# Kernel optimization log

Measured on AMD Instinct MI355X. Metric: run time of the kernel, lower is better.

The kernel has to match this reference:

```python
import jax, jax.numpy as jnp
import numpy as np

BATCH, SEQ, D_MODEL = 4, 4096, 1024
HEADS, DIM_HEAD = 8, 128
BUCKET, N_HASHES = 64, 4
N_BUCKETS = SEQ // BUCKET
LN_EPS = 1e-3
SELF_ATTN_VAL = -5e4   # TOKEN_SELF_ATTN_VALUE in reformer_pytorch
MASK_VAL = -1e9        # stand-in for max_neg_value on padded keys
UNIT_EPS = 1e-6        # make_unit_length epsilon


def setup_inputs() -> dict:
    key = jax.random.key(0)
    ks = jax.random.split(key, 8)
    s = 0.02
    return {
        "i": jax.random.normal(ks[0], (BATCH, SEQ, D_MODEL), jnp.float32),
        "mask": jnp.ones((BATCH, SEQ), dtype=bool),
        "rotations": jax.random.normal(ks[1], (DIM_HEAD, N_HASHES, N_BUCKETS // 2), jnp.float32),
        "Wqk": jax.random.normal(ks[2], (D_MODEL, D_MODEL), jnp.float32) * s,
        "Wv": jax.random.normal(ks[3], (D_MODEL, D_MODEL), jnp.float32) * s,
        "Wo": jax.random.normal(ks[4], (D_MODEL, D_MODEL), jnp.float32) * s,
        "bo": jnp.zeros((D_MODEL,), jnp.float32),
        "ln_g": jnp.ones((D_MODEL,), jnp.float32),
        "ln_b": jnp.zeros((D_MODEL,), jnp.float32),
    }


def _look_one_back(x):
    # concat each chunk with the previous chunk along the within-chunk axis
    return jnp.concatenate([x, jnp.roll(x, 1, axis=1)], axis=2)


def _lsh_attention(qk, v, mask, rotations):
    # qk, v: (B, T, d) with B = batch*heads; mask: (B, T) bool
    B, T, d = qk.shape
    # --- hash into buckets (no grad through hashing) ---
    rot = jnp.einsum('btd,dhr->bhtr', jax.lax.stop_gradient(qk), rotations)
    rot = jnp.concatenate([rot, -rot], axis=-1)              # (B, nh, T, n_buckets)
    buckets = jnp.argmax(rot, axis=-1)                       # (B, nh, T)
    offsets = (jnp.arange(N_HASHES) * N_BUCKETS)[None, :, None]
    buckets = (buckets + offsets).reshape(B, N_HASHES * T)
    # --- stable bucket sort of tokens ---
    ticker = jnp.arange(N_HASHES * T)
    buckets_and_t = buckets * T + (ticker % T)               # unique keys
    sticker = jnp.argsort(buckets_and_t, axis=-1)            # (B, nh*T)
    undo_sort = jnp.argsort(sticker, axis=-1)
    st = sticker % T                                         # original positions
    sqk = jnp.take_along_axis(qk, st[..., None], axis=1)
    sv = jnp.take_along_axis(v, st[..., None], axis=1)
    # --- chunked local attention ---
    n_chunks = N_HASHES * N_BUCKETS
    bq_t = st.reshape(B, n_chunks, BUCKET)
    bq = sqk.reshape(B, n_chunks, BUCKET, d)
    nrm = jnp.linalg.norm(bq, axis=-1, keepdims=True)
    bk = bq / jnp.maximum(nrm, UNIT_EPS)                     # shared-QK: keys are unit-length queries
    bv = sv.reshape(B, n_chunks, BUCKET, d)
    bk = _look_one_back(bk)                                  # (B, C, 2*BUCKET, d)
    bv = _look_one_back(bv)
    bkv_t = _look_one_back(bq_t)                             # (B, C, 2*BUCKET)
    dots = jnp.einsum('bcid,bcjd->bcij', bq, bk) * (d ** -0.5)
    # input (padding) mask
    mq = jnp.take_along_axis(mask, st, axis=1).reshape(B, n_chunks, BUCKET)
    mkv = _look_one_back(mq)
    dots = jnp.where(mq[..., :, None] & mkv[..., None, :], dots, MASK_VAL)
    # avoid attending to self except as a fallback
    dots = jnp.where(bq_t[..., :, None] == bkv_t[..., None, :], SELF_ATTN_VAL, dots)
    dots_lse = jax.nn.logsumexp(dots, axis=-1, keepdims=True)  # (B, C, BUCKET, 1)
    probs = jnp.exp(dots - dots_lse)
    bo = jnp.einsum('bcij,bcjd->bcid', probs, bv)
    so = bo.reshape(B, N_HASHES * T, d)
    slogits = dots_lse.reshape(B, N_HASHES * T)
    # --- unsort and combine hash rounds via softmax over per-round logsumexps ---
    o = jnp.take_along_axis(so, undo_sort[..., None], axis=1).reshape(B, N_HASHES, T, d)
    logits = jnp.take_along_axis(slogits, undo_sort, axis=1).reshape(B, N_HASHES, T, 1)
    w = jnp.exp(logits - jax.nn.logsumexp(logits, axis=1, keepdims=True))
    return jnp.sum(o * w, axis=1)                            # (B, T, d)


def _forward(i, mask, rotations, Wqk, Wv, Wo, bo, ln_g, ln_b):
    b, t, dm = i.shape
    qk = i @ Wqk
    v = i @ Wv

    def split_heads(x):
        return x.reshape(b, t, HEADS, DIM_HEAD).transpose(0, 2, 1, 3).reshape(b * HEADS, t, DIM_HEAD)

    qk, v = split_heads(qk), split_heads(v)
    m = jnp.repeat(mask, HEADS, axis=0)                      # (b*h, t)
    out = _lsh_attention(qk, v, m, rotations)
    out = out.reshape(b, HEADS, t, DIM_HEAD).transpose(0, 2, 1, 3).reshape(b, t, dm)
    out = out @ Wo + bo                                      # to_out
    # eval-mode dropout is identity; then LayerNorm(eps=1e-3)
    mu = out.mean(-1, keepdims=True)
    var = out.var(-1, keepdims=True)
    return (out - mu) / jnp.sqrt(var + LN_EPS) * ln_g + ln_b


def reference(i, mask, rotations, Wqk, Wv, Wo, bo, ln_g, ln_b):
    return _forward(i, mask, rotations, Wqk, Wv, Wo, bo, ln_g, ln_b)
```

## Files before the change

### kernel.cpp

```cpp
#include <hip/hip_runtime.h>
#include <hip/hip_bf16.h>

#define B_   4
#define T_   4096
#define DM   1024
#define H_   8
#define DH   128
#define BHN  32
#define NH   4
#define NB   64
#define NT   16384
#define NC   256
#define SCALE_ 0.08838834764831845f
#define SELF_VAL -50000.0f
#define FLAG_CAP 262144
#define GAP_THR 2.5e-3f

typedef unsigned short u16;
typedef __attribute__((ext_vector_type(8))) short short8;
typedef __attribute__((ext_vector_type(8))) unsigned short us8;
typedef __attribute__((ext_vector_type(4))) float f32x4;

__device__ __forceinline__ float bf2f(u16 x) {
  union { unsigned u; float f; } c; c.u = ((unsigned)x) << 16; return c.f;
}
__device__ __forceinline__ u16 f2bf(float f) {
  union { float f; unsigned u; } c; c.f = f;
  unsigned r = (c.u + 0x7FFFu + ((c.u >> 16) & 1u)) >> 16;
  return (u16)r;
}
__device__ __forceinline__ void gload16(const void* g, void* l) {
  __builtin_amdgcn_global_load_lds(
      (const __attribute__((address_space(1))) void*)g,
      (__attribute__((address_space(3))) void*)l, 16, 0, 0);
}

__global__ __launch_bounds__(256) void k_isplit(
    const float* __restrict__ I, u16* __restrict__ ih, u16* __restrict__ il) {
  size_t idx = ((size_t)blockIdx.x * 256 + threadIdx.x) * 8;
  us8 vh, vl;
  #pragma unroll
  for (int e = 0; e < 8; ++e) {
    float x = I[idx + e];
    u16 h = f2bf(x);
    vh[e] = h;
    vl[e] = f2bf(x - bf2f(h));
  }
  *(us8*)(ih + idx) = vh;
  *(us8*)(il + idx) = vl;
}

__global__ __launch_bounds__(256) void k_wr(
    const float* __restrict__ Wqk, const float* __restrict__ R, double* __restrict__ WR) {
  __shared__ float lR[128][128];
  int tid = threadIdx.x;
  int k0 = blockIdx.x * 64, h = blockIdx.y;
  #pragma unroll
  for (int q = 0; q < 64; ++q)
    ((float*)lR)[q * 256 + tid] = R[q * 256 + tid];
  __syncthreads();
  int k = k0 + (tid >> 2);
  int hr0 = (tid & 3) * 32;
  double acc[32];
  #pragma unroll
  for (int j = 0; j < 32; ++j) acc[j] = 0.0;
  for (int d = 0; d < 128; ++d) {
    double w = (double)Wqk[(size_t)k * DM + h * DH + d];
    #pragma unroll
    for (int j = 0; j < 32; ++j)
      acc[j] = fma(w, (double)lR[d][hr0 + j], acc[j]);
  }
  double* o = WR + ((size_t)h * 1024 + k) * 128 + hr0;
  #pragma unroll
  for (int j = 0; j < 32; ++j) o[j] = acc[j];
}

__global__ __launch_bounds__(256) void k_wsplit(
    const float* __restrict__ Wqk, const float* __restrict__ Wv,
    const float* __restrict__ Wo, const double* __restrict__ WR,
    u16* __restrict__ Wqkvt, u16* __restrict__ Wot, u16* __restrict__ WR2t) {
  int tid = blockIdx.x * 256 + threadIdx.x;
  int k = tid >> 7, n8 = (tid & 127) << 3;
  #pragma unroll
  for (int j = 0; j < 8; ++j) {
    int n = n8 + j;
    Wqkvt[(size_t)n * 1024 + k]          = f2bf(Wqk[(size_t)k * 1024 + n]);
    Wqkvt[(size_t)(1024 + n) * 1024 + k] = f2bf(Wv [(size_t)k * 1024 + n]);
    Wot  [(size_t)n * 1024 + k]          = f2bf(Wo [(size_t)k * 1024 + n]);
    double w = WR[((size_t)(n >> 7) * 1024 + k) * 128 + (n & 127)];
    u16 wh = f2bf((float)w);
    u16 wl = f2bf((float)(w - (double)bf2f(wh)));
    WR2t[(size_t)n * 2048 + k] = wh;
    WR2t[(size_t)n * 2048 + 1024 + k] = wl;
  }
}

__global__ void k_zero(unsigned* flagc) { if (threadIdx.x == 0) *flagc = 0; }

template <int EPI>
__global__ __launch_bounds__(256) void k_gemm(
    const u16* __restrict__ A, const u16* __restrict__ A2,
    const u16* __restrict__ Bt,
    u16* __restrict__ outb, u16* __restrict__ outb2,
    float* __restrict__ outf, const float* __restrict__ bias,
    int* __restrict__ buckets, unsigned* __restrict__ flagc, int* __restrict__ flags) {
  __shared__ char smem[34816];
  u16 (*smA)[64] = (u16 (*)[64])smem;
  u16 (*smB)[64] = (u16 (*)[64])(smem + 16384);
  int tid = threadIdx.x;
  int m0 = blockIdx.x * 128, n0 = blockIdx.y * 128;
  int w = tid >> 6, lane = tid & 63;
  int wr = w >> 1, wc = w & 1;
  int arow = lane & 15, kg = lane >> 4;
  const int ldb = (EPI == 2) ? 2048 : 1024;
  int lrow = lane >> 3;
  int gch = (lane & 7) ^ lrow;

  f32x4 acc[4][4];
  #pragma unroll
  for (int m = 0; m < 4; ++m)
    #pragma unroll
    for (int n = 0; n < 4; ++n) acc[m][n] = (f32x4){0.f, 0.f, 0.f, 0.f};

  int axor = (arow & 7) << 3;

  auto run_seg = [&](const u16* Ab, const u16* Bb) {
    for (int kk = 0; kk < 1024; kk += 64) {
      __syncthreads();
      #pragma unroll
      for (int q = 0; q < 4; ++q) {
        int row = q * 32 + w * 8 + lrow;
        gload16(Ab + (size_t)(m0 + row) * 1024 + kk + gch * 8,
                smem + (q * 4096 + w * 1024));
        gload16(Bb + (size_t)(n0 + row) * ldb + kk + gch * 8,
                smem + 16384 + (q * 4096 + w * 1024));
      }
      __syncthreads();
      #pragma unroll
      for (int ks = 0; ks < 2; ++ks) {
        short8 af[4], bf[4];
        #pragma unroll
        for (int m = 0; m < 4; ++m)
          af[m] = *(const short8*)(&smA[wr * 64 + m * 16 + arow][((ks * 4 + kg) << 3) ^ axor]);
        #pragma unroll
        for (int n = 0; n < 4; ++n)
          bf[n] = *(const short8*)(&smB[wc * 64 + n * 16 + arow][((ks * 4 + kg) << 3) ^ axor]);
        #pragma unroll
        for (int m = 0; m < 4; ++m)
          #pragma unroll
          for (int n = 0; n < 4; ++n)
            acc[m][n] = __builtin_amdgcn_mfma_f32_16x16x32_bf16(af[m], bf[n], acc[m][n], 0, 0, 0);
      }
    }
  };

  if constexpr (EPI == 2) {
    run_seg(A, Bt);
    run_seg(A, Bt + 1024);
    run_seg(A2, Bt);
  } else {
    run_seg(A, Bt);
  }

  if constexpr (EPI == 0) {
    u16* dst = (n0 < 1024) ? outb : outb2;
    int nc0 = (n0 < 1024) ? n0 : (n0 - 1024);
    #pragma unroll
    for (int m = 0; m < 4; ++m)
      #pragma unroll
      for (int n = 0; n < 4; ++n)
        #pragma unroll
        for (int r = 0; r < 4; ++r) {
          int orow = wr * 64 + m * 16 + kg * 4 + r;
          int ocol = wc * 64 + n * 16 + arow;
          dst[(size_t)(m0 + orow) * 1024 + nc0 + ocol] = f2bf(acc[m][n][r]);
        }
  } else if constexpr (EPI == 1) {
    #pragma unroll
    for (int m = 0; m < 4; ++m)
      #pragma unroll
      for (int n = 0; n < 4; ++n)
        #pragma unroll
        for (int r = 0; r < 4; ++r) {
          int orow = wr * 64 + m * 16 + kg * 4 + r;
          int ocol = wc * 64 + n * 16 + arow;
          outf[(size_t)(m0 + orow) * 1024 + n0 + ocol] = acc[m][n][r] + bias[n0 + ocol];
        }
  } else {
    float (*sC)[132] = (float (*)[132])smem;
    #pragma unroll
    for (int pass = 0; pass < 2; ++pass) {
      __syncthreads();
      if (wr == pass) {
        #pragma unroll
        for (int m = 0; m < 4; ++m)
          #pragma unroll
          for (int n = 0; n < 4; ++n)
            #pragma unroll
            for (int r = 0; r < 4; ++r)
              sC[m * 16 + kg * 4 + r][wc * 64 + n * 16 + arow] = acc[m][n][r];
      }
      __syncthreads();
      int tok = tid >> 2, hash = tid & 3;
      const float* rw = &sC[tok][hash * 32];
      float m1 = -3.4e38f, m2 = -3.4e38f; int bi = 0;
      #pragma unroll
      for (int j = 0; j < 32; ++j) {
        float vv = rw[j];
        if (vv > m1) { m2 = m1; m1 = vv; bi = j; }
        else if (vv > m2) m2 = vv;
      }
      #pragma unroll
      for (int j = 0; j < 32; ++j) {
        float vv = -rw[j];
        if (vv > m1) { m2 = m1; m1 = vv; bi = 32 + j; }
        else if (vv > m2) m2 = vv;
      }
      int bt = m0 + pass * 64 + tok;
      int b = bt >> 12, t = bt & 4095;
      buckets[((size_t)(b * 8 + blockIdx.y) * 4 + hash) * T_ + t] = bi;
      if (m1 - m2 < GAP_THR) {
        unsigned pos = atomicAdd(flagc, 1u);
        if (pos < FLAG_CAP) flags[pos] = (bt << 5) | ((int)blockIdx.y << 2) | hash;
      }
    }
  }
}

__global__ __launch_bounds__(64) void k_fb(
    const float* __restrict__ I, const double* __restrict__ WR,
    const unsigned* __restrict__ flagc, const int* __restrict__ flags,
    int* __restrict__ buckets) {
  unsigned n = *flagc; if (n > FLAG_CAP) n = FLAG_CAP;
  int lane = threadIdx.x;
  for (unsigned it = blockIdx.x; it < n; it += gridDim.x) {
    int f = flags[it];
    int bt = f >> 5, h = (f >> 2) & 7, hash = f & 3;
    int j = lane & 31, half = lane >> 5;
    const float* ip = I + (size_t)bt * 1024 + half * 512;
    const double* wp = WR + ((size_t)h * 1024 + half * 512) * 128 + hash * 32 + j;
    double acc = 0.0;
    for (int k = 0; k < 512; ++k)
      acc = fma((double)ip[k], wp[(size_t)k * 128], acc);
    acc += __shfl_down(acc, 32, 64);
    double bv = acc; int bi = j;
    double vneg = -acc;
    if (vneg > bv) { bv = vneg; bi = 32 + j; }
    #pragma unroll
    for (int m = 1; m < 32; m <<= 1) {
      double ov = __shfl_xor(bv, m, 64);
      int oi = __shfl_xor(bi, m, 64);
      if (ov > bv || (ov == bv && oi < bi)) { bv = ov; bi = oi; }
    }
    if (lane == 0) {
      int b = bt >> 12, t = bt & 4095;
      buckets[((size_t)(b * 8 + h) * 4 + hash) * T_ + t] = bi;
    }
  }
}

__global__ __launch_bounds__(64) void k_sort(
    const int* __restrict__ buckets, int* __restrict__ st) {
  __shared__ int hist[64][65];
  __shared__ int base[64];
  int bh = blockIdx.x, r = blockIdx.y;
  int m = threadIdx.x;
  #pragma unroll
  for (int b = 0; b < 64; ++b) hist[b][m] = 0;
  __syncthreads();
  const int* bk = buckets + ((size_t)bh * NH + r) * T_;
  for (int q = 0; q < 64; ++q) hist[bk[m * 64 + q]][m]++;
  __syncthreads();
  {
    int run = 0;
    for (int c = 0; c < 64; ++c) { int x = hist[m][c]; hist[m][c] = run; run += x; }
    base[m] = run;
  }
  __syncthreads();
  if (m == 0) {
    int s = 0;
    for (int b = 0; b < 64; ++b) { int x = base[b]; base[b] = s; s += x; }
  }
  __syncthreads();
  int* stb = st + (size_t)bh * NT + (size_t)r * T_;
  for (int q = 0; q < 64; ++q) {
    int t = m * 64 + q;
    int b = bk[t];
    int pos = base[b] + hist[b][m]++;
    stb[pos] = t;
  }
}

__global__ __launch_bounds__(256) void k_attn(
    const u16* __restrict__ qk, const u16* __restrict__ V, const int* __restrict__ st,
    u16* __restrict__ o_u, float* __restrict__ slog_u) {
  __shared__ u16 kbuf[128][136];
  __shared__ u16 pbuf[64][136];
  __shared__ int tks[128];
  float* psum   = (float*)&pbuf[0][0];
  float* recipn = (float*)&pbuf[4][0];
  int tid = threadIdx.x;
  int bh = blockIdx.x, chunk = blockIdx.y;
  int round = chunk >> 6;
  int bb_ = bh >> 3, hh_ = bh & 7;
  const int* stb = st + (size_t)bh * NT;
  if (tid < 128) {
    int j = tid;
    int p = (j < 64) ? (chunk * 64 + j)
                     : (((chunk + NC - 1) % NC) * 64 + (j - 64));
    tks[j] = stb[p];
  }
  __syncthreads();
  {
    int j = tid & 127, half = tid >> 7;
    const ushort4* rp = (const ushort4*)(qk + ((size_t)(bb_ * T_ + tks[j])) * DM + hh_ * DH + half * 64);
    ushort4* dp = (ushort4*)(&kbuf[j][half * 64]);
    float ss = 0.f;
    #pragma unroll
    for (int c = 0; c < 16; ++c) {
      ushort4 x = rp[c];
      float f0 = bf2f(x.x), f1 = bf2f(x.y), f2 = bf2f(x.z), f3 = bf2f(x.w);
      ss += f0 * f0 + f1 * f1 + f2 * f2 + f3 * f3;
      dp[c] = x;
    }
    psum[j * 2 + half] = ss;
  }
  __syncthreads();
  if (tid < 128) {
    float n = sqrtf(psum[tid * 2] + psum[tid * 2 + 1]);
    recipn[tid] = 1.f / fmaxf(n, 1e-6f);
  }
  __syncthreads();

  int w = tid >> 6, lane = tid & 63;
  int arow = lane & 15, kgrp = lane >> 4;

  f32x4 acc[8];
  #pragma unroll
  for (int n = 0; n < 8; ++n) acc[n] = (f32x4){0.f, 0.f, 0.f, 0.f};
  __builtin_amdgcn_s_setprio(1);
  #pragma unroll
  for (int kk = 0; kk < 4; ++kk) {
    short8 a = *(const short8*)(&kbuf[w * 16 + arow][kk * 32 + kgrp * 8]);
    #pragma unroll
    for (int n = 0; n < 8; ++n) {
      short8 bb = *(const short8*)(&kbuf[n * 16 + arow][kk * 32 + kgrp * 8]);
      acc[n] = __builtin_amdgcn_mfma_f32_16x16x32_bf16(a, bb, acc[n], 0, 0, 0);
    }
  }
  __builtin_amdgcn_s_setprio(0);

  int ti[4];
  #pragma unroll
  for (int r = 0; r < 4; ++r) ti[r] = tks[w * 16 + kgrp * 4 + r];
  float vals[8][4];
  float rmax[4] = {-3.0e38f, -3.0e38f, -3.0e38f, -3.0e38f};
  #pragma unroll
  for (int n = 0; n < 8; ++n) {
    int j = n * 16 + arow;
    float rc = recipn[j] * SCALE_;
    int tj = tks[j];
    #pragma unroll
    for (int r = 0; r < 4; ++r) {
      float d = acc[n][r] * rc;
      if (ti[r] == tj) d = SELF_VAL;
      vals[n][r] = d;
      rmax[r] = fmaxf(rmax[r], d);
    }
  }
  __syncthreads();
  #pragma unroll
  for (int m = 1; m <= 8; m <<= 1) {
    #pragma unroll
    for (int r = 0; r < 4; ++r) rmax[r] = fmaxf(rmax[r], __shfl_xor(rmax[r], m, 64));
  }
  float rsum[4] = {0.f, 0.f, 0.f, 0.f};
  #pragma unroll
  for (int n = 0; n < 8; ++n) {
    #pragma unroll
    for (int r = 0; r < 4; ++r) {
      float e = __expf(vals[n][r] - rmax[r]);
      vals[n][r] = e;
      rsum[r] += e;
    }
  }
  #pragma unroll
  for (int m = 1; m <= 8; m <<= 1) {
    #pragma unroll
    for (int r = 0; r < 4; ++r) rsum[r] += __shfl_xor(rsum[r], m, 64);
  }
  float rinv[4], lse[4];
  #pragma unroll
  for (int r = 0; r < 4; ++r) {
    rinv[r] = 1.f / rsum[r];
    lse[r] = rmax[r] + __logf(rsum[r]);
  }
  if (arow == 0) {
    #pragma unroll
    for (int r = 0; r < 4; ++r)
      slog_u[((size_t)(bh * NH + round)) * T_ + ti[r]] = lse[r];
  }
  #pragma unroll
  for (int n = 0; n < 8; ++n) {
    #pragma unroll
    for (int r = 0; r < 4; ++r)
      pbuf[w * 16 + kgrp * 4 + r][n * 16 + arow] = f2bf(vals[n][r] * rinv[r]);
  }
  __syncthreads();
  {
    int j = tid & 127, half = tid >> 7;
    const ushort4* rp = (const ushort4*)(V + ((size_t)(bb_ * T_ + tks[j])) * DM + hh_ * DH + half * 64);
    #pragma unroll
    for (int c = 0; c < 16; ++c) {
      ushort4 x = rp[c];
      int d = half * 64 + c * 4;
      kbuf[d + 0][j] = x.x;
      kbuf[d + 1][j] = x.y;
      kbuf[d + 2][j] = x.z;
      kbuf[d + 3][j] = x.w;
    }
  }
  __syncthreads();

  f32x4 acc2[8];
  #pragma unroll
  for (int n = 0; n < 8; ++n) acc2[n] = (f32x4){0.f, 0.f, 0.f, 0.f};
  __builtin_amdgcn_s_setprio(1);
  #pragma unroll
  for (int kk = 0; kk < 4; ++kk) {
    short8 a = *(const short8*)(&pbuf[w * 16 + arow][kk * 32 + kgrp * 8]);
    #pragma unroll
    for (int n = 0; n < 8; ++n) {
      short8 bb = *(const short8*)(&kbuf[n * 16 + arow][kk * 32 + kgrp * 8]);
      acc2[n] = __builtin_amdgcn_mfma_f32_16x16x32_bf16(a, bb, acc2[n], 0, 0, 0);
    }
  }
  __builtin_amdgcn_s_setprio(0);
  u16* ob = o_u + ((size_t)(bh * NH + round)) * T_ * DH;
  #pragma unroll
  for (int n = 0; n < 8; ++n) {
    #pragma unroll
    for (int r = 0; r < 4; ++r)
      ob[(size_t)ti[r] * DH + n * 16 + arow] = f2bf(acc2[n][r]);
  }
}

__global__ __launch_bounds__(256) void k_comb(
    const u16* __restrict__ o_u, const float* __restrict__ slog_u,
    u16* __restrict__ attn) {
  int tid = threadIdx.x;
  int bh = blockIdx.y;
  int t0 = blockIdx.x * 16;
  int dd = tid & 127;
  int b = bh >> 3, h = bh & 7;
  #pragma unroll
  for (int i = 0; i < 8; ++i) {
    int t = t0 + (tid >> 7) + i * 2;
    float l[4];
    #pragma unroll
    for (int r = 0; r < 4; ++r)
      l[r] = slog_u[((size_t)(bh * NH + r)) * T_ + t];
    float m = fmaxf(fmaxf(l[0], l[1]), fmaxf(l[2], l[3]));
    float wv[4]; float wsum = 0.f;
    #pragma unroll
    for (int r = 0; r < 4; ++r) { wv[r] = __expf(l[r] - m); wsum += wv[r]; }
    float rs = 1.f / wsum;
    float o = 0.f;
    #pragma unroll
    for (int r = 0; r < 4; ++r)
      o += wv[r] * bf2f(o_u[(((size_t)(bh * NH + r)) * T_ + t) * DH + dd]);
    o *= rs;
    attn[((size_t)(b * T_ + t)) * DM + h * DH + dd] = f2bf(o);
  }
}

__global__ __launch_bounds__(256) void k_ln(
    const float* __restrict__ X, const float* __restrict__ G,
    const float* __restrict__ Bt, float* __restrict__ out) {
  __shared__ float w1[4], w2[4];
  int row = blockIdx.x, tid = threadIdx.x;
  const float4 v = ((const float4*)(X + (size_t)row * DM))[tid];
  float s = v.x + v.y + v.z + v.w;
  float s2 = v.x * v.x + v.y * v.y + v.z * v.z + v.w * v.w;
  #pragma unroll
  for (int m = 1; m < 64; m <<= 1) {
    s += __shfl_xor(s, m, 64);
    s2 += __shfl_xor(s2, m, 64);
  }
  int wid = tid >> 6;
  if ((tid & 63) == 0) { w1[wid] = s; w2[wid] = s2; }
  __syncthreads();
  float S = w1[0] + w1[1] + w1[2] + w1[3];
  float S2 = w2[0] + w2[1] + w2[2] + w2[3];
  float mu = S * (1.f / DM);
  float var = S2 * (1.f / DM) - mu * mu;
  float inv = 1.0f / sqrtf(var + 1e-3f);
  float4 g = ((const float4*)G)[tid];
  float4 b = ((const float4*)Bt)[tid];
  float4 o;
  o.x = (v.x - mu) * inv * g.x + b.x;
  o.y = (v.y - mu) * inv * g.y + b.y;
  o.z = (v.z - mu) * inv * g.z + b.z;
  o.w = (v.w - mu) * inv * g.w + b.w;
  ((float4*)(out + (size_t)row * DM))[tid] = o;
}

extern "C" void kernel_launch(void* const* d_in, const int* in_sizes, int n_in,
                              void* d_out, int out_size, void* d_ws, size_t ws_size,
                              hipStream_t stream) {
  const float* I   = (const float*)d_in[0];
  const float* R   = (const float*)d_in[2];
  const float* Wqk = (const float*)d_in[3];
  const float* Wv  = (const float*)d_in[4];
  const float* Wo  = (const float*)d_in[5];
  const float* bo  = (const float*)d_in[6];
  const float* lng = (const float*)d_in[7];
  const float* lnb = (const float*)d_in[8];

  char* ws = (char*)d_ws;
  const size_t MB = 1ull << 20;
  u16*      qk      = (u16*)(ws + 0);
  u16*      v       = (u16*)(ws + 32 * MB);
  u16*      o_u     = (u16*)(ws + 64 * MB);
  u16*      i_hi    = (u16*)(ws + 64 * MB);
  u16*      i_lo    = (u16*)(ws + 96 * MB);
  double*   WR      = (double*)(ws + 128 * MB);
  int*      flags   = (int*)(ws + 136 * MB);
  unsigned* flagc   = (unsigned*)(ws + 137 * MB);
  int*      buckets = (int*)(ws + 138 * MB);
  u16*      Wqkvt   = (u16*)(ws + 140 * MB);
  u16*      WR2t    = (u16*)(ws + 144 * MB);
  float*    outp    = (float*)(ws + 64 * MB);
  int*      st      = (int*)(ws + 192 * MB);
  float*    slog_u  = (float*)(ws + 196 * MB);
  u16*      Wot     = (u16*)(ws + 198 * MB);
  u16*      attnb   = qk;
  float*    out     = (float*)d_out;

  k_isplit<<<8192, 256, 0, stream>>>(I, i_hi, i_lo);
  k_wr<<<dim3(16, 8), 256, 0, stream>>>(Wqk, R, WR);
  k_wsplit<<<512, 256, 0, stream>>>(Wqk, Wv, Wo, WR, Wqkvt, Wot, WR2t);
  k_zero<<<1, 64, 0, stream>>>(flagc);
  k_gemm<0><<<dim3(128, 16), 256, 0, stream>>>(i_hi, nullptr, Wqkvt, qk, v, nullptr, nullptr, nullptr, nullptr, nullptr);
  k_gemm<2><<<dim3(128, 8), 256, 0, stream>>>(i_hi, i_lo, WR2t, nullptr, nullptr, nullptr, nullptr, buckets, flagc, flags);
  k_fb<<<1024, 64, 0, stream>>>(I, WR, flagc, flags, buckets);
  k_sort<<<dim3(BHN, NH), 64, 0, stream>>>(buckets, st);
  k_attn<<<dim3(BHN, NC), 256, 0, stream>>>(qk, v, st, o_u, slog_u);
  k_comb<<<dim3(T_ / 16, BHN), 256, 0, stream>>>(o_u, slog_u, attnb);
  k_gemm<1><<<dim3(128, 8), 256, 0, stream>>>(attnb, nullptr, Wot, nullptr, nullptr, outp, bo, nullptr, nullptr, nullptr);
  k_ln<<<B_ * T_, 256, 0, stream>>>(outp, lng, lnb, out);
}
```

Before: 533.3 us.

## Precompute key norms once and overlap V loads with softmax in attention

Adds a kernel that computes the reciprocal L2 norm of every qk row per head once, so the attention kernel no longer recomputes norms for each of the 128 gathered rows in every chunk. The attention kernel now copies K with wider 16-byte loads and issues the V gather and transpose before the softmax reductions, which removes one barrier and lets the global loads overlap with the math. The flag-counter reset moves into k_wsplit, which drops one launch. In exchange it adds an extra pass over qk (8192 blocks) and a small normalization buffer in the workspace.

```diff
diff --git a/kernel.cpp b/kernel.cpp
--- a/kernel.cpp
+++ b/kernel.cpp
@@ -78,7 +78,9 @@
 __global__ __launch_bounds__(256) void k_wsplit(
     const float* __restrict__ Wqk, const float* __restrict__ Wv,
     const float* __restrict__ Wo, const double* __restrict__ WR,
-    u16* __restrict__ Wqkvt, u16* __restrict__ Wot, u16* __restrict__ WR2t) {
+    u16* __restrict__ Wqkvt, u16* __restrict__ Wot, u16* __restrict__ WR2t,
+    unsigned* __restrict__ flagc) {
+  if (blockIdx.x == 0 && threadIdx.x == 0) *flagc = 0;
   int tid = blockIdx.x * 256 + threadIdx.x;
   int k = tid >> 7, n8 = (tid & 127) << 3;
   #pragma unroll
@@ -95,7 +97,22 @@
   }
 }
 
-__global__ void k_zero(unsigned* flagc) { if (threadIdx.x == 0) *flagc = 0; }
+__global__ __launch_bounds__(256) void k_norm(
+    const u16* __restrict__ qk, float* __restrict__ rn) {
+  int tid = threadIdx.x;
+  int g = tid >> 4, l = tid & 15;
+  int row = blockIdx.x * 2 + (g >> 3), head = g & 7;
+  us8 x = *(const us8*)(qk + (size_t)row * DM + head * DH + l * 8);
+  float ss = 0.f;
+  #pragma unroll
+  for (int e = 0; e < 8; ++e) {
+    float f = bf2f((u16)x[e]);
+    ss += f * f;
+  }
+  #pragma unroll
+  for (int m = 1; m <= 8; m <<= 1) ss += __shfl_xor(ss, m, 64);
+  if (l == 0) rn[(size_t)row * 8 + head] = 1.f / fmaxf(sqrtf(ss), 1e-6f);
+}
 
 template <int EPI>
 __global__ __launch_bounds__(256) void k_gemm(
@@ -293,12 +310,11 @@
 
 __global__ __launch_bounds__(256) void k_attn(
     const u16* __restrict__ qk, const u16* __restrict__ V, const int* __restrict__ st,
-    u16* __restrict__ o_u, float* __restrict__ slog_u) {
+    const float* __restrict__ rn, u16* __restrict__ o_u, float* __restrict__ slog_u) {
   __shared__ u16 kbuf[128][136];
   __shared__ u16 pbuf[64][136];
   __shared__ int tks[128];
-  float* psum   = (float*)&pbuf[0][0];
-  float* recipn = (float*)&pbuf[4][0];
+  float* recipn = (float*)&pbuf[0][0];
   int tid = threadIdx.x;
   int bh = blockIdx.x, chunk = blockIdx.y;
   int round = chunk >> 6;
@@ -313,23 +329,12 @@
   __syncthreads();
   {
     int j = tid & 127, half = tid >> 7;
-    const ushort4* rp = (const ushort4*)(qk + ((size_t)(bb_ * T_ + tks[j])) * DM + hh_ * DH + half * 64);
-    ushort4* dp = (ushort4*)(&kbuf[j][half * 64]);
-    float ss = 0.f;
-    #pragma unroll
-    for (int c = 0; c < 16; ++c) {
-      ushort4 x = rp[c];
-      float f0 = bf2f(x.x), f1 = bf2f(x.y), f2 = bf2f(x.z), f3 = bf2f(x.w);
-      ss += f0 * f0 + f1 * f1 + f2 * f2 + f3 * f3;
-      dp[c] = x;
-    }
-    psum[j * 2 + half] = ss;
-  }
-  __syncthreads();
-  if (tid < 128) {
-    float n = sqrtf(psum[tid * 2] + psum[tid * 2 + 1]);
-    recipn[tid] = 1.f / fmaxf(n, 1e-6f);
-  }
+    const us8* rp = (const us8*)(qk + ((size_t)(bb_ * T_ + tks[j])) * DM + hh_ * DH + half * 64);
+    us8* dp = (us8*)(&kbuf[j][half * 64]);
+    #pragma unroll
+    for (int c = 0; c < 8; ++c) dp[c] = rp[c];
+  }
+  if (tid < 128) recipn[tid] = rn[(size_t)(bb_ * T_ + tks[tid]) * 8 + hh_];
   __syncthreads();
 
   int w = tid >> 6, lane = tid & 63;
@@ -369,6 +374,19 @@
     }
   }
   __syncthreads();
+
+  {
+    int j = tid & 127, half = tid >> 7;
+    const us8* rp = (const us8*)(V + ((size_t)(bb_ * T_ + tks[j])) * DM + hh_ * DH + half * 64);
+    #pragma unroll
+    for (int c = 0; c < 8; ++c) {
+      us8 x = rp[c];
+      int d = half * 64 + c * 8;
+      #pragma unroll
+      for (int e = 0; e < 8; ++e) kbuf[d + e][j] = (u16)x[e];
+    }
+  }
+
   #pragma unroll
   for (int m = 1; m <= 8; m <<= 1) {
     #pragma unroll
@@ -405,20 +423,6 @@
     #pragma unroll
     for (int r = 0; r < 4; ++r)
       pbuf[w * 16 + kgrp * 4 + r][n * 16 + arow] = f2bf(vals[n][r] * rinv[r]);
-  }
-  __syncthreads();
-  {
-    int j = tid & 127, half = tid >> 7;
-    const ushort4* rp = (const ushort4*)(V + ((size_t)(bb_ * T_ + tks[j])) * DM + hh_ * DH + half * 64);
-    #pragma unroll
-    for (int c = 0; c < 16; ++c) {
-      ushort4 x = rp[c];
-      int d = half * 64 + c * 4;
-      kbuf[d + 0][j] = x.x;
-      kbuf[d + 1][j] = x.y;
-      kbuf[d + 2][j] = x.z;
-      kbuf[d + 3][j] = x.w;
-    }
   }
   __syncthreads();
 
@@ -532,6 +536,7 @@
   u16*      WR2t    = (u16*)(ws + 144 * MB);
   float*    outp    = (float*)(ws + 64 * MB);
   int*      st      = (int*)(ws + 192 * MB);
+  float*    rn      = (float*)(ws + 194 * MB);
   float*    slog_u  = (float*)(ws + 196 * MB);
   u16*      Wot     = (u16*)(ws + 198 * MB);
   u16*      attnb   = qk;
@@ -539,13 +544,13 @@
 
   k_isplit<<<8192, 256, 0, stream>>>(I, i_hi, i_lo);
   k_wr<<<dim3(16, 8), 256, 0, stream>>>(Wqk, R, WR);
-  k_wsplit<<<512, 256, 0, stream>>>(Wqk, Wv, Wo, WR, Wqkvt, Wot, WR2t);
-  k_zero<<<1, 64, 0, stream>>>(flagc);
+  k_wsplit<<<512, 256, 0, stream>>>(Wqk, Wv, Wo, WR, Wqkvt, Wot, WR2t, flagc);
   k_gemm<0><<<dim3(128, 16), 256, 0, stream>>>(i_hi, nullptr, Wqkvt, qk, v, nullptr, nullptr, nullptr, nullptr, nullptr);
+  k_norm<<<8192, 256, 0, stream>>>(qk, rn);
   k_gemm<2><<<dim3(128, 8), 256, 0, stream>>>(i_hi, i_lo, WR2t, nullptr, nullptr, nullptr, nullptr, buckets, flagc, flags);
   k_fb<<<1024, 64, 0, stream>>>(I, WR, flagc, flags, buckets);
   k_sort<<<dim3(BHN, NH), 64, 0, stream>>>(buckets, st);
-  k_attn<<<dim3(BHN, NC), 256, 0, stream>>>(qk, v, st, o_u, slog_u);
+  k_attn<<<dim3(BHN, NC), 256, 0, stream>>>(qk, v, st, rn, o_u, slog_u);
   k_comb<<<dim3(T_ / 16, BHN), 256, 0, stream>>>(o_u, slog_u, attnb);
   k_gemm<1><<<dim3(128, 8), 256, 0, stream>>>(attnb, nullptr, Wot, nullptr, nullptr, outp, bo, nullptr, nullptr, nullptr);
   k_ln<<<B_ * T_, 256, 0, stream>>>(outp, lng, lnb, out);
```

After: 544.2 us. 1.02x slower.
